# Performance work log

Hardware: AMD Instinct MI355X
Metric: run time of the kernel (lower is better)

Reference implementation:

```python
import jax, jax.numpy as jnp
import numpy as np
from jax import lax

SD = 16  # sample_duration
POOL_KS = (SD, SD * 3 // 4, SD // 2, SD // 4)  # (16, 12, 8, 4)


def conv3d_same(x, w, b):
    # x: [B,C,T,H,W], w: [O,I,3,3,3]
    y = lax.conv_general_dilated(
        x, w, window_strides=(1, 1, 1), padding=[(1, 1), (1, 1), (1, 1)],
        dimension_numbers=("NCDHW", "OIDHW", "NCDHW"))
    return y + b[None, :, None, None, None]


def maxpool_t(x, k):
    # MaxPool3d((k,1,1), stride=1): max over sliding temporal window
    return lax.reduce_window(x, -jnp.inf, lax.max,
                             (1, 1, k, 1, 1), (1, 1, 1, 1, 1), "VALID")


def head1x1(x, w, b):
    # 1x1x1 Conv3d as einsum; x: [B,C,T,H,W], w: [O,C]
    return jnp.einsum("bcthw,oc->bothw", x, w) + b[None, :, None, None, None]


def cls_prob(score):
    # _RPN.reshape(x,2) -> softmax(dim=1) -> reshape back to [B,30,T,H,W]
    B, C, T, H, W = score.shape
    s2 = score.reshape(B, 2, (C * T) // 2, H, W)
    p = jax.nn.softmax(s2, axis=1)
    return p.reshape(B, C, T, H, W)


def setup_inputs() -> dict:
    key = jax.random.key(0)
    ks = jax.random.split(key, 12)
    din, B, H, W = 512, 2, 28, 28
    s = 0.05
    return {
        "base_feat": jax.random.normal(ks[0], (B, din, SD, H, W), jnp.float32),
        "im_info": jnp.ones((B, 3), jnp.float32) * 448.0,
        "gt_boxes": jax.random.uniform(ks[1], (B, 20, 5), jnp.float32),
        "gt_rois": jax.random.uniform(ks[2], (B, 20, SD, 5), jnp.float32),
        "W_conv": jax.random.normal(ks[3], (din, din, 3, 3, 3), jnp.float32) * 0.01,
        "b_conv": jnp.zeros((din,), jnp.float32),
        "W_cls": jax.random.normal(ks[4], (30, din), jnp.float32) * s,
        "b_cls": jnp.zeros((30,), jnp.float32),
        "W_bbox": jax.random.normal(ks[5], (960, din), jnp.float32) * s,
        "b_bbox": jnp.zeros((960,), jnp.float32),
        "W_bbox_34": jax.random.normal(ks[6], (720, din), jnp.float32) * s,
        "b_bbox_34": jnp.zeros((720,), jnp.float32),
        "W_bbox_2": jax.random.normal(ks[7], (480, din), jnp.float32) * s,
        "b_bbox_2": jnp.zeros((480,), jnp.float32),
        "W_bbox_4": jax.random.normal(ks[8], (240, din), jnp.float32) * s,
        "b_bbox_4": jnp.zeros((240,), jnp.float32),
    }


def reference(base_feat, im_info, gt_boxes, gt_rois,
              W_conv, b_conv, W_cls, b_cls,
              W_bbox, b_bbox, W_bbox_34, b_bbox_34,
              W_bbox_2, b_bbox_2, W_bbox_4, b_bbox_4):
    # RPN conv + relu
    x = jax.nn.relu(conv3d_same(base_feat, W_conv, b_conv))
    # four temporal max-pool branches (T' = 1, 5, 9, 13)
    pools = [maxpool_t(x, k) for k in POOL_KS]
    # NOTE: original code applies the SAME RPN_cls_score conv to all branches
    probs = tuple(cls_prob(head1x1(p, W_cls, b_cls)) for p in pools)
    bbox_ws = [(W_bbox, b_bbox), (W_bbox_34, b_bbox_34),
               (W_bbox_2, b_bbox_2), (W_bbox_4, b_bbox_4)]
    bboxes = tuple(head1x1(p, w, b) for p, (w, b) in zip(pools, bbox_ws))
    return probs + bboxes
```

## Files before the change

### kernel.cpp

```cpp
#include <hip/hip_runtime.h>

typedef unsigned short u16;
typedef unsigned int   u32;
typedef __bf16  bf16x8 __attribute__((ext_vector_type(8)));
typedef float   f32x4  __attribute__((ext_vector_type(4)));

__device__ __forceinline__ float bf2f(u16 u) {
    u32 v = ((u32)u) << 16;
    return __builtin_bit_cast(float, v);
}
__device__ __forceinline__ u16 f2bf(float f) {
    u32 u = __builtin_bit_cast(u32, f);
    return (u16)((u + 0x7FFFu + ((u >> 16) & 1u)) >> 16);
}
__device__ __forceinline__ float ldf(const void* p, long i, int f32) {
    return f32 ? ((const float*)p)[i] : bf2f(((const u16*)p)[i]);
}
__device__ __forceinline__ void gl2lds16(const u16* g, u16* l) {
    __builtin_amdgcn_global_load_lds(
        (const __attribute__((address_space(1))) void*)g,
        (__attribute__((address_space(3))) void*)l, 16, 0, 0);
}

__global__ void detect_dtype(const u32* __restrict__ im, int* __restrict__ flag)
{
    if (blockIdx.x == 0 && threadIdx.x == 0)
        *flag = (im[0] == 0x43E00000u) ? 1 : 0;
}

__global__ void zero_kernel(uint4* __restrict__ p, const int n)
{
    int i = blockIdx.x * 256 + threadIdx.x;
    if (i < n) p[i] = uint4{0u, 0u, 0u, 0u};
}

__global__ void pad_fill(const void* __restrict__ src, u16* __restrict__ xpad,
                         const int* __restrict__ flag)
{
    const int f32 = *flag;
    __shared__ u16 lds[56 * 40];
    int blk = blockIdx.x;
    const int h2  = blk % 14;  blk /= 14;
    const int c32 = blk & 15;  blk >>= 4;
    const int t   = blk & 15;
    const int b   = blk >> 4;
    const int tid = threadIdx.x;
    const long sbase = ((long)(b * 512 + c32 * 32) * 16 + t) * 784 + h2 * 56;
    #pragma unroll
    for (int it = tid; it < 1792; it += 256) {
        const int c = it / 56, p = it - c * 56;
        float v = f32 ? ((const float*)src)[sbase + (long)c * 12544 + p]
                      : bf2f(((const u16*)src)[sbase + (long)c * 12544 + p]);
        lds[p * 40 + c] = f2bf(v);
    }
    __syncthreads();
    if (tid < 224) {
        const int p = tid >> 2, g = tid & 3;
        const int h = h2 * 2 + p / 28, w = p % 28;
        const long o = (((long)(b * 18 + t + 1) * 30 + h + 1) * 30 + (w + 1)) * 512
                       + c32 * 32 + g * 8;
        *(uint4*)&xpad[o] = *(const uint4*)&lds[p * 40 + g * 8];
    }
}

__global__ void wt_transform(const void* __restrict__ wconv, u16* __restrict__ wt,
                             const int* __restrict__ flag)
{
    const int f32 = *flag;
    __shared__ u16 lds[256 * 28];
    const int tid = threadIdx.x;
    const int pair_base = blockIdx.x * 256;
    const long s0 = (long)pair_base * 27;
    for (int it = tid; it < 256 * 27; it += 256) {
        const int p = it / 27, o = it - p * 27;
        float v = f32 ? ((const float*)wconv)[s0 + it]
                      : bf2f(((const u16*)wconv)[s0 + it]);
        lds[p * 28 + o] = f2bf(v);
    }
    __syncthreads();
    #pragma unroll
    for (int off = 0; off < 27; ++off)
        wt[(long)off * 262144 + pair_base + tid] = lds[tid * 28 + off];
}

__global__ void cvt_heads(const void* s0, const void* s1, const void* s2,
                          const void* s3, const void* s4,
                          u16* __restrict__ dst, const int* __restrict__ flag)
{
    const int f32 = *flag;
    int i = blockIdx.x * 256 + threadIdx.x;
    if (i >= 1244160) return;
    const void* s; long j;
    if      (i < 15360)   { s = s0; j = i; }
    else if (i < 506880)  { s = s1; j = i - 15360; }
    else if (i < 875520)  { s = s2; j = i - 506880; }
    else if (i < 1121280) { s = s3; j = i - 875520; }
    else                  { s = s4; j = i - 1121280; }
    dst[i] = f2bf(ldf(s, j, f32));
}

__global__ void cvt_bias(const void* s0, const void* s1, const void* s2,
                         const void* s3, const void* s4, const void* s5,
                         float* __restrict__ dst, const int* __restrict__ flag)
{
    const int f32 = *flag;
    int i = blockIdx.x * 256 + threadIdx.x;
    if (i >= 2942) return;
    float v;
    if      (i < 512)  v = ldf(s0, i, f32);
    else if (i < 542)  v = ldf(s1, i - 512, f32);
    else if (i < 1502) v = ldf(s2, i - 542, f32);
    else if (i < 2222) v = ldf(s3, i - 1502, f32);
    else if (i < 2702) v = ldf(s4, i - 2222, f32);
    else               v = ldf(s5, i - 2702, f32);
    dst[i] = v;
}

__global__ __launch_bounds__(512, 2) void conv_gemm256(
    const u16* __restrict__ xpad, const u16* __restrict__ wt,
    const float* __restrict__ bfs, u16* __restrict__ y)
{
    __shared__ u16 smem[65536];
    const int tid = threadIdx.x;

    const int bx  = blockIdx.x;
    const int xcd = bx & 7, pos = bx >> 3;
    const int L   = (xcd < 4 ? xcd * 25 : 100 + (xcd - 4) * 24) + pos;
    const int m_base = (L & 1) * 256;
    const int n_base = (L >> 1) * 256;

    const int rq  = tid >> 2;
    const int gsw = (((tid & 3) ^ ((tid >> 3) & 3))) * 8;
    const u16* pa0 = wt + (long)(m_base + rq) * 512 + gsw;
    const u16* pa1 = pa0 + 128 * 512;

    const int n0 = n_base + rq;
    const int n1 = n0 + 128;
    int b0 = n0 / 12544, r0 = n0 % 12544;
    int t0 = r0 / 784,   q0 = r0 % 784;
    int h0 = q0 / 28,    w0 = q0 % 28;
    int b1 = n1 / 12544, r1 = n1 % 12544;
    int t1 = r1 / 784,   q1 = r1 % 784;
    int h1 = q1 / 28,    w1 = q1 % 28;
    const int sa0 = ((b0 * 18 + t0) * 30 + h0) * 30 + w0;
    const int sa1 = ((b1 * 18 + t1) * 30 + h1) * 30 + w1;
    const u16* pb0 = xpad + (long)sa0 * 512 + gsw;
    const u16* pb1 = xpad + (long)sa1 * 512 + gsw;

    const int lane = tid & 63, wid = tid >> 6;
    const int l16 = lane & 15, quad = lane >> 4;
    const int wm = wid >> 2;
    const int wn = wid & 3;
    const int slot  = (quad ^ ((l16 >> 1) & 3)) * 8;
    const int aoffs = (wm * 128 + l16) * 32 + slot;
    const int boffs = 8192 + (wn * 64 + l16) * 32 + slot;

    f32x4 acc[8][4] = {};

    #pragma unroll
    for (int k = 0; k < 3; ++k) {
        u16* dst = smem + (k << 14);
        gl2lds16(pa0 + k * 32, dst + tid * 8);
        gl2lds16(pa1 + k * 32, dst + 4096  + tid * 8);
        gl2lds16(pb0 + k * 32, dst + 8192  + tid * 8);
        gl2lds16(pb1 + k * 32, dst + 12288 + tid * 8);
    }
    asm volatile("s_waitcnt vmcnt(8)" ::: "memory");
    asm volatile("s_barrier" ::: "memory");

#define KTILE(ktl, STG)                                                        \
    {                                                                          \
        const u16* buf = smem + (((ktl) & 3) << 14);                           \
        long aoff = 0, boff = 0;                                               \
        u16* dst = nullptr;                                                    \
        if (STG) {                                                             \
            const int kts = (ktl) + 3;                                         \
            const int tap = kts >> 4, kc = kts & 15;                           \
            const int kd = tap / 9, r9 = tap - kd * 9;                         \
            const int kh = r9 / 3,  kw = r9 - kh * 3;                          \
            aoff = (long)tap * 262144 + kc * 32;                               \
            boff = (long)(kd * 900 + kh * 30 + kw) * 512 + kc * 32;            \
            dst  = smem + ((kts & 3) << 14);                                   \
        }                                                                      \
        bf16x8 af[4], bfr[4];                                                  \
        _Pragma("unroll")                                                      \
        for (int mi = 0; mi < 4; ++mi)                                         \
            af[mi] = *(const bf16x8*)&buf[aoffs + mi * 512];                   \
        _Pragma("unroll")                                                      \
        for (int ni = 0; ni < 4; ++ni)                                         \
            bfr[ni] = *(const bf16x8*)&buf[boffs + ni * 512];                  \
        if (STG) {                                                             \
            gl2lds16(pa0 + aoff, dst + tid * 8);                               \
            gl2lds16(pa1 + aoff, dst + 4096 + tid * 8);                        \
        }                                                                      \
        asm volatile("s_barrier" ::: "memory");                                \
        __builtin_amdgcn_s_setprio(1);                                         \
        _Pragma("unroll")                                                      \
        for (int mi = 0; mi < 4; ++mi)                                         \
            _Pragma("unroll")                                                  \
            for (int ni = 0; ni < 4; ++ni)                                     \
                acc[mi][ni] = __builtin_amdgcn_mfma_f32_16x16x32_bf16(         \
                    af[mi], bfr[ni], acc[mi][ni], 0, 0, 0);                    \
        __builtin_amdgcn_s_setprio(0);                                         \
        asm volatile("s_barrier" ::: "memory");                                \
        _Pragma("unroll")                                                      \
        for (int mi = 0; mi < 4; ++mi)                                         \
            af[mi] = *(const bf16x8*)&buf[aoffs + (mi + 4) * 512];             \
        if (STG) {                                                             \
            gl2lds16(pb0 + boff, dst + 8192  + tid * 8);                       \
            gl2lds16(pb1 + boff, dst + 12288 + tid * 8);                       \
            asm volatile("s_waitcnt vmcnt(8)" ::: "memory");                   \
        }                                                                      \
        asm volatile("s_barrier" ::: "memory");                                \
        __builtin_amdgcn_s_setprio(1);                                         \
        _Pragma("unroll")                                                      \
        for (int mi = 0; mi < 4; ++mi)                                         \
            _Pragma("unroll")                                                  \
            for (int ni = 0; ni < 4; ++ni)                                     \
                acc[mi + 4][ni] = __builtin_amdgcn_mfma_f32_16x16x32_bf16(     \
                    af[mi], bfr[ni], acc[mi + 4][ni], 0, 0, 0);                \
        __builtin_amdgcn_s_setprio(0);                                         \
        asm volatile("s_barrier" ::: "memory");                                \
    }

    for (int kt = 0; kt < 429; ++kt) KTILE(kt, 1)
    asm volatile("s_waitcnt vmcnt(0)" ::: "memory");
    asm volatile("s_barrier" ::: "memory");
    for (int kt = 429; kt < 432; ++kt) KTILE(kt, 0)
#undef KTILE

    #pragma unroll
    for (int mi = 0; mi < 8; ++mi) {
        const int mrow = m_base + wm * 128 + mi * 16 + quad * 4;
        float bias[4];
        #pragma unroll
        for (int r = 0; r < 4; ++r) bias[r] = bfs[mrow + r];
        #pragma unroll
        for (int ni = 0; ni < 4; ++ni) {
            const int ng = n_base + wn * 64 + ni * 16 + l16;
            f32x4 a = acc[mi][ni];
            u16 o0 = f2bf(fmaxf(a[0] + bias[0], 0.f));
            u16 o1 = f2bf(fmaxf(a[1] + bias[1], 0.f));
            u16 o2 = f2bf(fmaxf(a[2] + bias[2], 0.f));
            u16 o3 = f2bf(fmaxf(a[3] + bias[3], 0.f));
            uint2 pv;
            pv.x = (u32)o0 | ((u32)o1 << 16);
            pv.y = (u32)o2 | ((u32)o3 << 16);
            *(uint2*)&y[(long)ng * 512 + mrow] = pv;
        }
    }
}

__device__ __forceinline__ uint4 max8(uint4 A, uint4 Bv)
{
    const u16* a = (const u16*)&A;
    const u16* b = (const u16*)&Bv;
    uint4 R;
    u16* r = (u16*)&R;
    #pragma unroll
    for (int i = 0; i < 8; ++i) r[i] = (bf2f(a[i]) >= bf2f(b[i])) ? a[i] : b[i];
    return R;
}

__global__ void pool4_kernel(const u16* __restrict__ y, u16* __restrict__ p4)
{
    int g = blockIdx.x * 256 + threadIdx.x;
    if (g >= 2 * 13 * 784 * 64) return;
    const int c8 = g & 63;
    int pos = g >> 6;
    const int hw = pos % 784; pos /= 784;
    const int t0 = pos % 13; const int b = pos / 13;
    const u16* src = y + ((long)((b * 16 + t0) * 784 + hw)) * 512 + c8 * 8;
    uint4 v0 = *(const uint4*)(src);
    uint4 v1 = *(const uint4*)(src + 401408);
    uint4 v2 = *(const uint4*)(src + 802816);
    uint4 v3 = *(const uint4*)(src + 1204224);
    uint4 m = max8(max8(v0, v1), max8(v2, v3));
    *(uint4*)&p4[((long)((b * 13 + t0) * 784 + hw)) * 512 + c8 * 8] = m;
}

__global__ void pools2(const u16* __restrict__ p4, u16* __restrict__ p8,
                       u16* __restrict__ p12, u16* __restrict__ p16)
{
    int g = blockIdx.x * 256 + threadIdx.x;
    if (g >= 1505280) return;
    int Td; u16* dst; int nwin;
    if (g < 903168)       { Td = 9; dst = p8;  nwin = 2; }
    else if (g < 1404928) { g -= 903168;  Td = 5; dst = p12; nwin = 3; }
    else                  { g -= 1404928; Td = 1; dst = p16; nwin = 4; }
    const int c8 = g & 63;
    int pos = g >> 6;
    const int hw = pos % 784; pos /= 784;
    const int t = pos % Td; const int b = pos / Td;
    const u16* src = p4 + ((long)((b * 13 + t) * 784 + hw)) * 512 + c8 * 8;
    uint4 m = *(const uint4*)(src);
    #pragma unroll 3
    for (int j = 1; j < nwin; ++j)
        m = max8(m, *(const uint4*)(src + (long)j * 4 * 784 * 512));
    *(uint4*)&dst[((long)((b * Td + t) * 784 + hw)) * 512 + c8 * 8] = m;
}

__global__ __launch_bounds__(256, 2) void heads_gemm(
    const u16* __restrict__ p16, const u16* __restrict__ p12,
    const u16* __restrict__ p8,  const u16* __restrict__ p4,
    const u16* __restrict__ wcls, const u16* __restrict__ wb1,
    const u16* __restrict__ wb34, const u16* __restrict__ wb2,
    const u16* __restrict__ wb4,  const float* __restrict__ bfs,
    float* __restrict__ clsr, void* __restrict__ outv,
    const int* __restrict__ flag)
{
    const int f32 = *flag;
    int bid = blockIdx.x;
    const u16* pool; const u16* wbp; int Ti, CH, nt, mt; long boff, coff, ooff;
    if (bid < 104)      {             nt = bid % 13;  mt = bid / 13;  pool = p16; wbp = wb1;  Ti = 1;  CH = 960; boff = 542;  coff = 0;      ooff = 1317120; }
    else if (bid < 476) { bid -= 104; nt = bid % 62;  mt = bid / 62;  pool = p12; wbp = wb34; Ti = 5;  CH = 720; boff = 1502; coff = 47040;  ooff = 2822400; }
    else if (bid < 920) { bid -= 476; nt = bid % 111; mt = bid / 111; pool = p8;  wbp = wb2;  Ti = 9;  CH = 480; boff = 2222; coff = 282240; ooff = 8467200; }
    else                { bid -= 920; nt = bid % 160; mt = bid / 160; pool = p4;  wbp = wb4;  Ti = 13; CH = 240; boff = 2702; coff = 705600; ooff = 15240960; }
    const int M = 30 + CH;
    const int THW = Ti * 784;
    const int N = 2 * THW;
    const int n_base = nt * 128;
    const int m_base = mt * 128;

    __shared__ u16 lds_a[128 * 64];
    __shared__ u16 lds_b[128 * 64];
    const int tid = threadIdx.x;
    const int lane = tid & 63;
    const int wid  = tid >> 6;
    const int quad = lane >> 4;
    const int l16  = lane & 15;
    const int wm = (wid & 1) * 64;
    const int wn = (wid >> 1) * 64;
    const int srow = tid >> 3;
    const int lc8  = ((tid & 7) ^ (srow & 7)) * 8;

    const u16* arow[4]; const u16* brow[4];
    #pragma unroll
    for (int j = 0; j < 4; ++j) {
        int m = m_base + j * 32 + srow; if (m > M - 1) m = M - 1;
        arow[j] = ((m < 30) ? (wcls + m * 512) : (wbp + (m - 30) * 512)) + lc8;
        int n = n_base + j * 32 + srow; if (n > N - 1) n = N - 1;
        brow[j] = pool + (long)n * 512 + lc8;
    }

    u16* ldst_a = &lds_a[tid * 8];
    u16* ldst_b = &lds_b[tid * 8];

    int rowA[4], rowB[4];
    #pragma unroll
    for (int i = 0; i < 4; ++i) {
        rowA[i] = (wm + i * 16 + l16) * 64;
        rowB[i] = (wn + i * 16 + l16) * 64;
    }
    const int cx  = l16 & 7;
    const int ch0 = (quad ^ cx) * 8;
    const int ch1 = ((4 + quad) ^ cx) * 8;

    f32x4 acc[4][4] = {};
    for (int kc = 0; kc < 8; ++kc) {
        const int kcol = kc * 64;
        #pragma unroll
        for (int j = 0; j < 4; ++j)
            gl2lds16(arow[j] + kcol, ldst_a + j * 2048);
        #pragma unroll
        for (int j = 0; j < 4; ++j)
            gl2lds16(brow[j] + kcol, ldst_b + j * 2048);
        __syncthreads();
        #pragma unroll
        for (int h = 0; h < 2; ++h) {
            const int co = h ? ch1 : ch0;
            bf16x8 af[4], bfr[4];
            #pragma unroll
            for (int mi = 0; mi < 4; ++mi)
                af[mi]  = *(const bf16x8*)&lds_a[rowA[mi] + co];
            #pragma unroll
            for (int ni = 0; ni < 4; ++ni)
                bfr[ni] = *(const bf16x8*)&lds_b[rowB[ni] + co];
            #pragma unroll
            for (int mi = 0; mi < 4; ++mi)
                #pragma unroll
                for (int ni = 0; ni < 4; ++ni)
                    acc[mi][ni] = __builtin_amdgcn_mfma_f32_16x16x32_bf16(
                        af[mi], bfr[ni], acc[mi][ni], 0, 0, 0);
        }
        __syncthreads();
    }
    const float* bcls = bfs + 512;
    const float* bb   = bfs + boff;
    #pragma unroll
    for (int mi = 0; mi < 4; ++mi) {
        const int mrow = m_base + wm + mi * 16 + quad * 4;
        #pragma unroll
        for (int ni = 0; ni < 4; ++ni) {
            const int ng = n_base + wn + ni * 16 + l16;
            if (ng >= N) continue;
            const int b  = ng / THW;
            const int rr = ng % THW;
            f32x4 a = acc[mi][ni];
            #pragma unroll
            for (int r = 0; r < 4; ++r) {
                const int m = mrow + r;
                if (m >= M) break;
                const float bias = (m < 30) ? bcls[m] : bb[m - 30];
                const float v = a[r] + bias;
                if (m < 30) {
                    clsr[coff + ((long)(b * 30 + m)) * THW + rr] = v;
                } else {
                    const long oi = ooff + ((long)(b * CH + (m - 30))) * THW + rr;
                    if (f32) ((float*)outv)[oi] = v;
                    else     ((u16*)outv)[oi]   = f2bf(v);
                }
            }
        }
    }
}

__global__ void softmax_all(const float* __restrict__ clsr,
                            void* __restrict__ outv, const int* __restrict__ flag)
{
    const int f32 = *flag;
    int g = blockIdx.x * 256 + threadIdx.x;
    if (g >= 658560) return;
    int Ti; long off;
    if      (g < 23520)  { Ti = 1;  off = 0; }
    else if (g < 141120) { Ti = 5;  off = 47040;  g -= 23520; }
    else if (g < 352800) { Ti = 9;  off = 282240; g -= 141120; }
    else                 { Ti = 13; off = 705600; g -= 352800; }
    const int THW = Ti * 784;
    const int rr = g % THW;
    int r2 = g / THW;
    const int j = r2 % 15; const int b = r2 / 15;
    const long i0 = off + ((long)(b * 30 + j)) * THW + rr;
    const long i1 = off + ((long)(b * 30 + j + 15)) * THW + rr;
    const float s0 = clsr[i0], s1 = clsr[i1];
    const float mx = fmaxf(s0, s1);
    const float e0 = __expf(s0 - mx), e1 = __expf(s1 - mx);
    const float inv = 1.0f / (e0 + e1);
    if (f32) {
        ((float*)outv)[i0] = e0 * inv;
        ((float*)outv)[i1] = e1 * inv;
    } else {
        ((u16*)outv)[i0] = f2bf(e0 * inv);
        ((u16*)outv)[i1] = f2bf(e1 * inv);
    }
}

extern "C" void kernel_launch(void* const* d_in, const int* in_sizes, int n_in,
                              void* d_out, int out_size, void* d_ws, size_t ws_size,
                              hipStream_t stream)
{
    const void* base_feat = d_in[0];
    const u32*  im_info   = (const u32*)d_in[1];
    const void* W_conv    = d_in[4];
    const void* b_conv    = d_in[5];
    const void* W_cls     = d_in[6];
    const void* b_cls     = d_in[7];
    const void* W_bbox    = d_in[8];
    const void* b_bbox    = d_in[9];
    const void* W_bbox34  = d_in[10];
    const void* b_bbox34  = d_in[11];
    const void* W_bbox2   = d_in[12];
    const void* b_bbox2   = d_in[13];
    const void* W_bbox4   = d_in[14];
    const void* b_bbox4   = d_in[15];

    char* ws = (char*)d_ws;
    u16*   xpad = (u16*)  (ws + 0);
    u16*   wt   = (u16*)  (ws + 33177600);
    u16*   y    = (u16*)  (ws + 47333376);
    u16*   p4   = (u16*)  (ws + 73023488);
    u16*   p8   = (u16*)  (ws + 93896704);
    u16*   p12  = (u16*)  (ws + 108347392);
    u16*   p16  = (u16*)  (ws + 116375552);
    float* clsr = (float*)(ws + 117981184);
    int*   flag = (int*)  (ws + 123249664);
    u16*   whd  = (u16*)  (ws + 123249728);
    float* bfs  = (float*)(ws + 125738048);

    u16* w_cls_b  = whd;
    u16* w_b1_b   = whd + 15360;
    u16* w_b34_b  = whd + 506880;
    u16* w_b2_b   = whd + 875520;
    u16* w_b4_b   = whd + 1121280;

    detect_dtype<<<1, 64, 0, stream>>>(im_info, flag);
    zero_kernel<<<8100, 256, 0, stream>>>((uint4*)xpad, 2073600);
    pad_fill<<<7168, 256, 0, stream>>>(base_feat, xpad, flag);
    wt_transform<<<1024, 256, 0, stream>>>(W_conv, wt, flag);
    cvt_heads<<<4860, 256, 0, stream>>>(W_cls, W_bbox, W_bbox34, W_bbox2, W_bbox4,
                                        whd, flag);
    cvt_bias<<<12, 256, 0, stream>>>(b_conv, b_cls, b_bbox, b_bbox34, b_bbox2,
                                     b_bbox4, bfs, flag);

    conv_gemm256<<<196, 512, 0, stream>>>(xpad, wt, bfs, y);

    pool4_kernel<<<5096, 256, 0, stream>>>(y, p4);
    pools2<<<5880, 256, 0, stream>>>(p4, p8, p12, p16);

    heads_gemm<<<1400, 256, 0, stream>>>(p16, p12, p8, p4,
                                         w_cls_b, w_b1_b, w_b34_b, w_b2_b, w_b4_b,
                                         bfs, clsr, d_out, flag);

    softmax_all<<<2573, 256, 0, stream>>>(clsr, d_out, flag);
}
```

Baseline: 638.2 us.

## Collapse per-k-tile barriers into a single gated barrier per pipelined tile

Restructures the main GEMM loop of the implicit-GEMM conv. Each k-tile now has one vmcnt wait plus one barrier at its start, instead of four barriers split across two half-tile phases. All eight A fragments and four B fragments are read from LDS up front. All four global-to-LDS prefetch loads for tile kt+3 are then issued together, and the two MFMA halves run back-to-back. The drain tail uses decreasing vmcnt gates (8, 4, 0). The aim is to cut barrier stalls and give the MFMA stream a longer uninterrupted run, at the cost of more live VGPRs for fragments.

```diff
diff --git a/kernel.cpp b/kernel.cpp
--- a/kernel.cpp
+++ b/kernel.cpp
@@ -165,35 +165,35 @@
         gl2lds16(pb0 + k * 32, dst + 8192  + tid * 8);
         gl2lds16(pb1 + k * 32, dst + 12288 + tid * 8);
     }
-    asm volatile("s_waitcnt vmcnt(8)" ::: "memory");
-    asm volatile("s_barrier" ::: "memory");
-
-#define KTILE(ktl, STG)                                                        \
+
+#define KTILE(ktl, STG, GATE)                                                  \
     {                                                                          \
+        asm volatile("s_waitcnt vmcnt(" #GATE ")" ::: "memory");               \
+        asm volatile("s_barrier" ::: "memory");                                \
         const u16* buf = smem + (((ktl) & 3) << 14);                           \
-        long aoff = 0, boff = 0;                                               \
-        u16* dst = nullptr;                                                    \
-        if (STG) {                                                             \
-            const int kts = (ktl) + 3;                                         \
-            const int tap = kts >> 4, kc = kts & 15;                           \
-            const int kd = tap / 9, r9 = tap - kd * 9;                         \
-            const int kh = r9 / 3,  kw = r9 - kh * 3;                          \
-            aoff = (long)tap * 262144 + kc * 32;                               \
-            boff = (long)(kd * 900 + kh * 30 + kw) * 512 + kc * 32;            \
-            dst  = smem + ((kts & 3) << 14);                                   \
-        }                                                                      \
-        bf16x8 af[4], bfr[4];                                                  \
+        bf16x8 af[8], bfr[4];                                                  \
         _Pragma("unroll")                                                      \
         for (int mi = 0; mi < 4; ++mi)                                         \
             af[mi] = *(const bf16x8*)&buf[aoffs + mi * 512];                   \
         _Pragma("unroll")                                                      \
         for (int ni = 0; ni < 4; ++ni)                                         \
             bfr[ni] = *(const bf16x8*)&buf[boffs + ni * 512];                  \
+        _Pragma("unroll")                                                      \
+        for (int mi = 4; mi < 8; ++mi)                                         \
+            af[mi] = *(const bf16x8*)&buf[aoffs + mi * 512];                   \
         if (STG) {                                                             \
+            const int kts = (ktl) + 3;                                         \
+            const int tap = kts >> 4, kc = kts & 15;                           \
+            const int kd = tap / 9, r9 = tap - kd * 9;                         \
+            const int kh = r9 / 3,  kw = r9 - kh * 3;                          \
+            const long aoff = (long)tap * 262144 + kc * 32;                    \
+            const long boff = (long)(kd * 900 + kh * 30 + kw) * 512 + kc * 32; \
+            u16* dst = smem + ((kts & 3) << 14);                               \
             gl2lds16(pa0 + aoff, dst + tid * 8);                               \
-            gl2lds16(pa1 + aoff, dst + 4096 + tid * 8);                        \
+            gl2lds16(pa1 + aoff, dst + 4096  + tid * 8);                       \
+            gl2lds16(pb0 + boff, dst + 8192  + tid * 8);                       \
+            gl2lds16(pb1 + boff, dst + 12288 + tid * 8);                       \
         }                                                                      \
-        asm volatile("s_barrier" ::: "memory");                                \
         __builtin_amdgcn_s_setprio(1);                                         \
         _Pragma("unroll")                                                      \
         for (int mi = 0; mi < 4; ++mi)                                         \
@@ -201,32 +201,19 @@
             for (int ni = 0; ni < 4; ++ni)                                     \
                 acc[mi][ni] = __builtin_amdgcn_mfma_f32_16x16x32_bf16(         \
                     af[mi], bfr[ni], acc[mi][ni], 0, 0, 0);                    \
-        __builtin_amdgcn_s_setprio(0);                                         \
-        asm volatile("s_barrier" ::: "memory");                                \
         _Pragma("unroll")                                                      \
-        for (int mi = 0; mi < 4; ++mi)                                         \
-            af[mi] = *(const bf16x8*)&buf[aoffs + (mi + 4) * 512];             \
-        if (STG) {                                                             \
-            gl2lds16(pb0 + boff, dst + 8192  + tid * 8);                       \
-            gl2lds16(pb1 + boff, dst + 12288 + tid * 8);                       \
-            asm volatile("s_waitcnt vmcnt(8)" ::: "memory");                   \
-        }                                                                      \
-        asm volatile("s_barrier" ::: "memory");                                \
-        __builtin_amdgcn_s_setprio(1);                                         \
-        _Pragma("unroll")                                                      \
-        for (int mi = 0; mi < 4; ++mi)                                         \
+        for (int mi = 4; mi < 8; ++mi)                                         \
             _Pragma("unroll")                                                  \
             for (int ni = 0; ni < 4; ++ni)                                     \
-                acc[mi + 4][ni] = __builtin_amdgcn_mfma_f32_16x16x32_bf16(     \
-                    af[mi], bfr[ni], acc[mi + 4][ni], 0, 0, 0);                \
+                acc[mi][ni] = __builtin_amdgcn_mfma_f32_16x16x32_bf16(         \
+                    af[mi], bfr[ni], acc[mi][ni], 0, 0, 0);                    \
         __builtin_amdgcn_s_setprio(0);                                         \
-        asm volatile("s_barrier" ::: "memory");                                \
-    }
-
-    for (int kt = 0; kt < 429; ++kt) KTILE(kt, 1)
-    asm volatile("s_waitcnt vmcnt(0)" ::: "memory");
-    asm volatile("s_barrier" ::: "memory");
-    for (int kt = 429; kt < 432; ++kt) KTILE(kt, 0)
+    }
+
+    for (int kt = 0; kt < 429; ++kt) KTILE(kt, 1, 8)
+    KTILE(429, 0, 8)
+    KTILE(430, 0, 4)
+    KTILE(431, 0, 0)
 #undef KTILE
 
     #pragma unroll
```

New measurement: 582.4 us. 8.7% less time.
